# Performance work log

Hardware: AMD Instinct MI355X
Metric: run time of the kernel (lower is better)

The kernel has to match this reference:

```python
import jax, jax.numpy as jnp
import numpy as np

INPUT_DIM = 1024
OUTPUT_DIM = 1024
SPLINE_POINTS = 4

def setup_inputs() -> dict:
    key = jax.random.key(0)
    k1, k2 = jax.random.split(key)
    x = jax.random.normal(k1, (4096, INPUT_DIM), dtype=jnp.float32)
    spline_coeffs = jax.random.normal(k2, (OUTPUT_DIM, INPUT_DIM, SPLINE_POINTS, 4), dtype=jnp.float32)
    return {"x": x, "spline_coeffs": spline_coeffs}

def reference(x, spline_coeffs):
    # Per-feature min-max normalization over the batch dim (as in the torch code,
    # where x[:, j].min()/max() are taken over the batch).
    xmin = jnp.min(x, axis=0, keepdims=True)   # [1, D]
    xmax = jnp.max(x, axis=0, keepdims=True)
    xn = (x - xmin) / (xmax - xmin)            # [B, D]

    # The original sums the cubic polynomial over all spline_points, so the
    # effective coefficients are the sum over the spline_points axis.
    c = jnp.sum(spline_coeffs, axis=2)         # [O, D, 4]

    x2 = xn * xn
    x3 = x2 * xn
    # out[b, o] = sum_d c0*x^3 + c1*x^2 + c2*x + c3
    out = (jnp.einsum('bd,od->bo', x3, c[..., 0])
           + jnp.einsum('bd,od->bo', x2, c[..., 1])
           + jnp.einsum('bd,od->bo', xn, c[..., 2])
           + jnp.sum(c[..., 3], axis=1)[None, :])
    return out
```

## Files before the change

kernel.cpp:

```cpp
#include <hip/hip_runtime.h>
#include <hip/hip_bf16.h>
#include <stdint.h>
#include <stddef.h>

typedef __bf16 bf16;
typedef __attribute__((ext_vector_type(4))) __bf16 bf16x4;
typedef __attribute__((ext_vector_type(8))) __bf16 bf16x8;
typedef __attribute__((ext_vector_type(4))) float f32x4;

#define BATCH 4096
#define DIM 1024
#define ODIM 1024
#define K3 3072

#define WS_P      0
#define WS_CB     25165824
#define WS_BIAS   31457280
#define WS_PMIN   31461376
#define WS_PMAX   32509952
#define WS_MINV   33558528
#define WS_SCALE  33562624

#define ASYNC16(g, l)                                                          \
  __builtin_amdgcn_global_load_lds(                                            \
      (__attribute__((address_space(1))) void*)(g),                            \
      (__attribute__((address_space(3))) void*)(l), 16, 0, 0)

#define WAIT_VM(n) __builtin_amdgcn_s_waitcnt(0x0F00 | 0x0070 | ((n)&15) | ((((n)>>4)&3)<<14))
#define BARRIER()                     \
  do {                                \
    asm volatile("" ::: "memory");    \
    __builtin_amdgcn_s_barrier();     \
    asm volatile("" ::: "memory");    \
  } while (0)

__global__ void k_minmax_part(const float* __restrict__ x,
                              float* __restrict__ pmin,
                              float* __restrict__ pmax) {
  const int t = threadIdx.x;
  const int ch = blockIdx.x;
  const float* p = x + (size_t)ch * 16 * DIM + (t << 2);
  f32x4 mn = {1e30f, 1e30f, 1e30f, 1e30f};
  f32x4 mx = {-1e30f, -1e30f, -1e30f, -1e30f};
#pragma unroll
  for (int r = 0; r < 16; ++r) {
    f32x4 v = *(const f32x4*)(p + (size_t)r * DIM);
#pragma unroll
    for (int j = 0; j < 4; ++j) {
      mn[j] = fminf(mn[j], v[j]);
      mx[j] = fmaxf(mx[j], v[j]);
    }
  }
  *(f32x4*)(pmin + ch * DIM + (t << 2)) = mn;
  *(f32x4*)(pmax + ch * DIM + (t << 2)) = mx;
}

__global__ void k_minmax_final(const float* __restrict__ pmin,
                               const float* __restrict__ pmax,
                               float* __restrict__ minv,
                               float* __restrict__ scale) {
  int col = blockIdx.x * 256 + threadIdx.x;
  float mn = 1e30f, mx = -1e30f;
#pragma unroll 8
  for (int ch = 0; ch < 256; ++ch) {
    mn = fminf(mn, pmin[ch * DIM + col]);
    mx = fmaxf(mx, pmax[ch * DIM + col]);
  }
  minv[col] = mn;
  scale[col] = 1.0f / (mx - mn);
}

__global__ void k_prep(const float* __restrict__ x,
                       const float* __restrict__ minv,
                       const float* __restrict__ scale,
                       bf16* __restrict__ P,
                       const float* __restrict__ sp,
                       bf16* __restrict__ CB,
                       float* __restrict__ bias) {
  __shared__ float red[4];
  const int t = threadIdx.x;
  if (blockIdx.x < (BATCH / 2)) {
    const int b = blockIdx.x * 2 + (t >> 7);
    const int d = (t & 127) << 3;
    f32x4 xv0 = *(const f32x4*)(x + (size_t)b * DIM + d);
    f32x4 xv1 = *(const f32x4*)(x + (size_t)b * DIM + d + 4);
    f32x4 mn0 = *(const f32x4*)(minv + d);
    f32x4 mn1 = *(const f32x4*)(minv + d + 4);
    f32x4 sc0 = *(const f32x4*)(scale + d);
    f32x4 sc1 = *(const f32x4*)(scale + d + 4);
    bf16x8 o3, o2, o1;
#pragma unroll
    for (int j = 0; j < 4; ++j) {
      float xn = (xv0[j] - mn0[j]) * sc0[j];
      float x2 = xn * xn;
      float x3 = x2 * xn;
      o3[j] = (bf16)x3;
      o2[j] = (bf16)x2;
      o1[j] = (bf16)xn;
      float yn = (xv1[j] - mn1[j]) * sc1[j];
      float y2 = yn * yn;
      float y3 = y2 * yn;
      o3[j + 4] = (bf16)y3;
      o2[j + 4] = (bf16)y2;
      o1[j + 4] = (bf16)yn;
    }
    size_t base = (size_t)b * K3 + d;
    *(bf16x8*)(P + base) = o3;
    *(bf16x8*)(P + base + 1024) = o2;
    *(bf16x8*)(P + base + 2048) = o1;
  } else {
    const int o = blockIdx.x - (BATCH / 2);
    const int d = t << 2;
    f32x4 s[4];
#pragma unroll
    for (int dd = 0; dd < 4; ++dd) {
      const float* p = sp + ((size_t)o * DIM + d + dd) * 16;
      f32x4 acc = *(const f32x4*)(p);
      acc += *(const f32x4*)(p + 4);
      acc += *(const f32x4*)(p + 8);
      acc += *(const f32x4*)(p + 12);
      s[dd] = acc;
    }
    size_t cb = (size_t)o * K3 + d;
    bf16x4 c0 = {(bf16)s[0][0], (bf16)s[1][0], (bf16)s[2][0], (bf16)s[3][0]};
    bf16x4 c1 = {(bf16)s[0][1], (bf16)s[1][1], (bf16)s[2][1], (bf16)s[3][1]};
    bf16x4 c2 = {(bf16)s[0][2], (bf16)s[1][2], (bf16)s[2][2], (bf16)s[3][2]};
    *(bf16x4*)(CB + cb) = c0;
    *(bf16x4*)(CB + cb + 1024) = c1;
    *(bf16x4*)(CB + cb + 2048) = c2;
    float v = s[0][3] + s[1][3] + s[2][3] + s[3][3];
#pragma unroll
    for (int off = 32; off > 0; off >>= 1) v += __shfl_down(v, off, 64);
    int lane = t & 63, w = t >> 6;
    if (lane == 0) red[w] = v;
    __syncthreads();
    if (t == 0) bias[o] = red[0] + red[1] + red[2] + red[3];
  }
}

#define BM 128
#define BN 128
#define BKE 64
#define NIT (K3 / BKE)
#define NBUF 4
__global__ __launch_bounds__(256, 1) void k_gemm(const bf16* __restrict__ P,
                                                 const bf16* __restrict__ CBm,
                                                 const float* __restrict__ bias,
                                                 float* __restrict__ out) {
  __shared__ bf16 ldsm[NBUF][2][BM * BKE];

  const int tid = threadIdx.x;
  const int wave = tid >> 6;
  const int lane = tid & 63;

  const int f = blockIdx.x;
  const int chunk = f & 7;
  const int idx = f >> 3;
  const int mt = ((chunk >> 1) << 3) + (idx >> 2);
  const int nt = ((chunk & 1) << 2) + (idx & 3);
  const int bm = mt * BM;
  const int bn = nt * BN;

  const int wr = (wave >> 1) * 64;
  const int wc = (wave & 1) * 64;

  const size_t rowbytes = (size_t)K3 * 2;

  const char* gAp[4];
  const char* gBp[4];
  int ldso[4];
#pragma unroll
  for (int i = 0; i < 4; ++i) {
    int off = i * 4096 + tid * 16;
    int row = off >> 7;
    int q = (off >> 4) & 7;
    int gb = (q ^ (row & 7)) * 16;
    gAp[i] = (const char*)P + (size_t)(bm + row) * rowbytes + gb;
    gBp[i] = (const char*)CBm + (size_t)(bn + row) * rowbytes + gb;
    ldso[i] = i * 4096 + wave * 1024;
  }

  f32x4 acc[4][4] = {};

  const int mrow = lane & 15;
  const int kq = lane >> 4;

#define STAGE(buf, kt)                                                        \
  do {                                                                        \
    const size_t kb_ = (size_t)(kt) * (BKE * 2);                              \
    char* lA_ = (char*)&ldsm[buf][0][0];                                      \
    char* lB_ = (char*)&ldsm[buf][1][0];                                      \
    _Pragma("unroll") for (int i_ = 0; i_ < 4; ++i_)                          \
        ASYNC16(gAp[i_] + kb_, lA_ + ldso[i_]);                               \
    _Pragma("unroll") for (int i_ = 0; i_ < 4; ++i_)                          \
        ASYNC16(gBp[i_] + kb_, lB_ + ldso[i_]);                               \
  } while (0)

#define COMPUTE(buf)                                                          \
  do {                                                                        \
    const bf16* sA_ = &ldsm[buf][0][0];                                       \
    const bf16* sB_ = &ldsm[buf][1][0];                                       \
    _Pragma("unroll") for (int ks = 0; ks < 2; ++ks) {                        \
      bf16x8 af[4], bg[4];                                                    \
      _Pragma("unroll") for (int i = 0; i < 4; ++i) {                         \
        int row = wr + i * 16 + mrow;                                         \
        int sq = (ks * 4 + kq) ^ (row & 7);                                   \
        af[i] = *(const bf16x8*)&sA_[row * BKE + sq * 8];                     \
      }                                                                       \
      _Pragma("unroll") for (int j = 0; j < 4; ++j) {                         \
        int row = wc + j * 16 + mrow;                                         \
        int sq = (ks * 4 + kq) ^ (row & 7);                                   \
        bg[j] = *(const bf16x8*)&sB_[row * BKE + sq * 8];                     \
      }                                                                       \
      _Pragma("unroll") for (int i = 0; i < 4; ++i)                           \
          _Pragma("unroll") for (int j = 0; j < 4; ++j)                       \
              acc[i][j] = __builtin_amdgcn_mfma_f32_16x16x32_bf16(            \
                  af[i], bg[j], acc[i][j], 0, 0, 0);                          \
    }                                                                         \
  } while (0)

  STAGE(0, 0);
  STAGE(1, 1);
  STAGE(2, 2);
#pragma unroll 4
  for (int kt = 0; kt < NIT - 3; ++kt) {
    STAGE((kt + 3) & 3, kt + 3);
    WAIT_VM(24);
    BARRIER();
    COMPUTE(kt & 3);
    BARRIER();
  }
  WAIT_VM(16);
  BARRIER();
  COMPUTE(1);
  BARRIER();
  WAIT_VM(8);
  BARRIER();
  COMPUTE(2);
  BARRIER();
  WAIT_VM(0);
  BARRIER();
  COMPUTE(3);

  const int ccol = lane & 15;
  const int crow = (lane >> 4) * 4;
#pragma unroll
  for (int j = 0; j < 4; ++j) {
    const int col = bn + wc + j * 16 + ccol;
    const float bv = bias[col];
#pragma unroll
    for (int i = 0; i < 4; ++i) {
      const int row0 = bm + wr + i * 16 + crow;
#pragma unroll
      for (int r = 0; r < 4; ++r)
        out[(size_t)(row0 + r) * ODIM + col] = acc[i][j][r] + bv;
    }
  }
#undef STAGE
#undef COMPUTE
}

extern "C" void kernel_launch(void* const* d_in, const int* in_sizes, int n_in,
                              void* d_out, int out_size, void* d_ws, size_t ws_size,
                              hipStream_t stream) {
  (void)in_sizes; (void)n_in; (void)out_size; (void)ws_size;
  const float* x = (const float*)d_in[0];
  const float* sp = (const float*)d_in[1];
  float* out = (float*)d_out;
  char* ws = (char*)d_ws;

  bf16* Pm = (bf16*)(ws + WS_P);
  bf16* CBm = (bf16*)(ws + WS_CB);
  float* bias = (float*)(ws + WS_BIAS);
  float* pmin = (float*)(ws + WS_PMIN);
  float* pmax = (float*)(ws + WS_PMAX);
  float* minv = (float*)(ws + WS_MINV);
  float* scale = (float*)(ws + WS_SCALE);

  k_minmax_part<<<256, 256, 0, stream>>>(x, pmin, pmax);
  k_minmax_final<<<4, 256, 0, stream>>>(pmin, pmax, minv, scale);
  k_prep<<<(BATCH / 2) + ODIM, 256, 0, stream>>>(x, minv, scale, Pm, sp, CBm, bias);
  k_gemm<<<256, 256, 0, stream>>>(Pm, CBm, bias, out);
}
```

Baseline: 168.7 us.

## Overlap coefficient reduction with min-max partials; parallelize final min-max reduce

```diff
diff --git a/kernel.cpp b/kernel.cpp
--- a/kernel.cpp
+++ b/kernel.cpp
@@ -34,82 +34,32 @@
     asm volatile("" ::: "memory");    \
   } while (0)
 
-__global__ void k_minmax_part(const float* __restrict__ x,
-                              float* __restrict__ pmin,
-                              float* __restrict__ pmax) {
-  const int t = threadIdx.x;
-  const int ch = blockIdx.x;
-  const float* p = x + (size_t)ch * 16 * DIM + (t << 2);
-  f32x4 mn = {1e30f, 1e30f, 1e30f, 1e30f};
-  f32x4 mx = {-1e30f, -1e30f, -1e30f, -1e30f};
-#pragma unroll
-  for (int r = 0; r < 16; ++r) {
-    f32x4 v = *(const f32x4*)(p + (size_t)r * DIM);
-#pragma unroll
-    for (int j = 0; j < 4; ++j) {
-      mn[j] = fminf(mn[j], v[j]);
-      mx[j] = fmaxf(mx[j], v[j]);
-    }
-  }
-  *(f32x4*)(pmin + ch * DIM + (t << 2)) = mn;
-  *(f32x4*)(pmax + ch * DIM + (t << 2)) = mx;
-}
-
-__global__ void k_minmax_final(const float* __restrict__ pmin,
-                               const float* __restrict__ pmax,
-                               float* __restrict__ minv,
-                               float* __restrict__ scale) {
-  int col = blockIdx.x * 256 + threadIdx.x;
-  float mn = 1e30f, mx = -1e30f;
-#pragma unroll 8
-  for (int ch = 0; ch < 256; ++ch) {
-    mn = fminf(mn, pmin[ch * DIM + col]);
-    mx = fmaxf(mx, pmax[ch * DIM + col]);
-  }
-  minv[col] = mn;
-  scale[col] = 1.0f / (mx - mn);
-}
-
-__global__ void k_prep(const float* __restrict__ x,
-                       const float* __restrict__ minv,
-                       const float* __restrict__ scale,
-                       bf16* __restrict__ P,
-                       const float* __restrict__ sp,
-                       bf16* __restrict__ CB,
-                       float* __restrict__ bias) {
+__global__ void k_stream(const float* __restrict__ x,
+                         float* __restrict__ pmin,
+                         float* __restrict__ pmax,
+                         const float* __restrict__ sp,
+                         bf16* __restrict__ CB,
+                         float* __restrict__ bias) {
   __shared__ float red[4];
   const int t = threadIdx.x;
-  if (blockIdx.x < (BATCH / 2)) {
-    const int b = blockIdx.x * 2 + (t >> 7);
-    const int d = (t & 127) << 3;
-    f32x4 xv0 = *(const f32x4*)(x + (size_t)b * DIM + d);
-    f32x4 xv1 = *(const f32x4*)(x + (size_t)b * DIM + d + 4);
-    f32x4 mn0 = *(const f32x4*)(minv + d);
-    f32x4 mn1 = *(const f32x4*)(minv + d + 4);
-    f32x4 sc0 = *(const f32x4*)(scale + d);
-    f32x4 sc1 = *(const f32x4*)(scale + d + 4);
-    bf16x8 o3, o2, o1;
-#pragma unroll
-    for (int j = 0; j < 4; ++j) {
-      float xn = (xv0[j] - mn0[j]) * sc0[j];
-      float x2 = xn * xn;
-      float x3 = x2 * xn;
-      o3[j] = (bf16)x3;
-      o2[j] = (bf16)x2;
-      o1[j] = (bf16)xn;
-      float yn = (xv1[j] - mn1[j]) * sc1[j];
-      float y2 = yn * yn;
-      float y3 = y2 * yn;
-      o3[j + 4] = (bf16)y3;
-      o2[j + 4] = (bf16)y2;
-      o1[j + 4] = (bf16)yn;
+  if (blockIdx.x < 256) {
+    const int ch = blockIdx.x;
+    const float* p = x + (size_t)ch * 16 * DIM + (t << 2);
+    f32x4 mn = {1e30f, 1e30f, 1e30f, 1e30f};
+    f32x4 mx = {-1e30f, -1e30f, -1e30f, -1e30f};
+#pragma unroll
+    for (int r = 0; r < 16; ++r) {
+      f32x4 v = *(const f32x4*)(p + (size_t)r * DIM);
+#pragma unroll
+      for (int j = 0; j < 4; ++j) {
+        mn[j] = fminf(mn[j], v[j]);
+        mx[j] = fmaxf(mx[j], v[j]);
+      }
     }
-    size_t base = (size_t)b * K3 + d;
-    *(bf16x8*)(P + base) = o3;
-    *(bf16x8*)(P + base + 1024) = o2;
-    *(bf16x8*)(P + base + 2048) = o1;
+    *(f32x4*)(pmin + ch * DIM + (t << 2)) = mn;
+    *(f32x4*)(pmax + ch * DIM + (t << 2)) = mx;
   } else {
-    const int o = blockIdx.x - (BATCH / 2);
+    const int o = blockIdx.x - 256;
     const int d = t << 2;
     f32x4 s[4];
 #pragma unroll
@@ -136,6 +86,67 @@
     __syncthreads();
     if (t == 0) bias[o] = red[0] + red[1] + red[2] + red[3];
   }
+}
+
+__global__ void k_minmax_final(const float* __restrict__ pmin,
+                               const float* __restrict__ pmax,
+                               float* __restrict__ minv,
+                               float* __restrict__ scale) {
+  __shared__ float smn[4][64], smx[4][64];
+  const int t = threadIdx.x;
+  const int lane = t & 63;
+  const int w = t >> 6;
+  const int col = blockIdx.x * 64 + lane;
+  float mn = 1e30f, mx = -1e30f;
+#pragma unroll 8
+  for (int ch = w; ch < 256; ch += 4) {
+    mn = fminf(mn, pmin[ch * DIM + col]);
+    mx = fmaxf(mx, pmax[ch * DIM + col]);
+  }
+  smn[w][lane] = mn;
+  smx[w][lane] = mx;
+  __syncthreads();
+  if (w == 0) {
+    mn = fminf(fminf(smn[0][lane], smn[1][lane]), fminf(smn[2][lane], smn[3][lane]));
+    mx = fmaxf(fmaxf(smx[0][lane], smx[1][lane]), fmaxf(smx[2][lane], smx[3][lane]));
+    minv[col] = mn;
+    scale[col] = 1.0f / (mx - mn);
+  }
+}
+
+__global__ void k_powers(const float* __restrict__ x,
+                         const float* __restrict__ minv,
+                         const float* __restrict__ scale,
+                         bf16* __restrict__ P) {
+  const int t = threadIdx.x;
+  const int b = blockIdx.x * 2 + (t >> 7);
+  const int d = (t & 127) << 3;
+  f32x4 xv0 = *(const f32x4*)(x + (size_t)b * DIM + d);
+  f32x4 xv1 = *(const f32x4*)(x + (size_t)b * DIM + d + 4);
+  f32x4 mn0 = *(const f32x4*)(minv + d);
+  f32x4 mn1 = *(const f32x4*)(minv + d + 4);
+  f32x4 sc0 = *(const f32x4*)(scale + d);
+  f32x4 sc1 = *(const f32x4*)(scale + d + 4);
+  bf16x8 o3, o2, o1;
+#pragma unroll
+  for (int j = 0; j < 4; ++j) {
+    float xn = (xv0[j] - mn0[j]) * sc0[j];
+    float x2 = xn * xn;
+    float x3 = x2 * xn;
+    o3[j] = (bf16)x3;
+    o2[j] = (bf16)x2;
+    o1[j] = (bf16)xn;
+    float yn = (xv1[j] - mn1[j]) * sc1[j];
+    float y2 = yn * yn;
+    float y3 = y2 * yn;
+    o3[j + 4] = (bf16)y3;
+    o2[j + 4] = (bf16)y2;
+    o1[j + 4] = (bf16)yn;
+  }
+  size_t base = (size_t)b * K3 + d;
+  *(bf16x8*)(P + base) = o3;
+  *(bf16x8*)(P + base + 1024) = o2;
+  *(bf16x8*)(P + base + 2048) = o1;
 }
 
 #define BM 128
@@ -277,8 +288,8 @@
   float* minv = (float*)(ws + WS_MINV);
   float* scale = (float*)(ws + WS_SCALE);
 
-  k_minmax_part<<<256, 256, 0, stream>>>(x, pmin, pmax);
-  k_minmax_final<<<4, 256, 0, stream>>>(pmin, pmax, minv, scale);
-  k_prep<<<(BATCH / 2) + ODIM, 256, 0, stream>>>(x, minv, scale, Pm, sp, CBm, bias);
+  k_stream<<<1280, 256, 0, stream>>>(x, pmin, pmax, sp, CBm, bias);
+  k_minmax_final<<<16, 256, 0, stream>>>(pmin, pmax, minv, scale);
+  k_powers<<<2048, 256, 0, stream>>>(x, minv, scale, Pm);
   k_gemm<<<256, 256, 0, stream>>>(Pm, CBm, bias, out);
 }
```

After: 155.6 us. 7.8% less time.
